# Performance work log

Hardware: AMD Instinct MI355X
Metric: run time of the kernel (lower is better)

The kernel has to match this reference:

```python
import jax, jax.numpy as jnp
import numpy as np

B, T, D, H, K, V, W = 2, 2048, 1024, 16, 64, 64, 256
BANK = 64
CUE = 50250
EPS = 1e-6
SCALE = K ** -0.5
LOCAL_SCALE = 0.3
ROPE_BASE = 10000.0


def setup_inputs() -> dict:
    key = jax.random.key(0)
    ks = jax.random.split(key, 13)
    s = 0.02
    return {
        "x": jax.random.normal(ks[0], (B, T, D), jnp.float32),
        "gdn_state": jax.random.normal(ks[1], (B, H, K, V), jnp.float32),
        "input_ids": jax.random.randint(ks[2], (B, T), 0, 50320),
        "key_bank": jax.random.normal(ks[3], (H, BANK, K), jnp.float32),
        "norm_w": jnp.ones((D,), jnp.float32),
        "wq": jax.random.normal(ks[4], (D, D), jnp.float32) * s,
        "wk": jax.random.normal(ks[5], (D, D), jnp.float32) * s,
        "wv": jax.random.normal(ks[6], (D, D), jnp.float32) * s,
        "wo": jax.random.normal(ks[7], (D, D), jnp.float32) * s,
        "w_gq": jax.random.normal(ks[8], (H * K, D), jnp.float32) * s,
        "w_ro": jax.random.normal(ks[9], (D, H * V), jnp.float32) * s,
        "w_gate": jax.random.normal(ks[10], (H, D), jnp.float32) * s,
        "b_gate": jnp.ones((H,), jnp.float32),
    }


def _rope(u):
    # u: [B, T, H, K]
    inv_freq = 1.0 / (ROPE_BASE ** (jnp.arange(0, K, 2, dtype=jnp.float32) / K))
    t = jnp.arange(T, dtype=jnp.float32)
    freqs = t[:, None] * inv_freq[None, :]            # [T, K/2]
    emb = jnp.concatenate([freqs, freqs], axis=-1)    # [T, K]
    cos = jnp.cos(emb)[None, :, None, :]
    sin = jnp.sin(emb)[None, :, None, :]
    u1, u2 = u[..., : K // 2], u[..., K // 2 :]
    rotated = jnp.concatenate([-u2, u1], axis=-1)
    return u * cos + rotated * sin


def reference(x, gdn_state, input_ids, key_bank, norm_w, wq, wk, wv, wo,
              w_gq, w_ro, w_gate, b_gate):
    # RMSNorm
    rms = jnp.sqrt(jnp.mean(x * x, axis=-1, keepdims=True) + EPS)
    x_norm = x / rms * norm_w

    # QKV projections -> [B, T, H, K]
    q = (x_norm @ wq.T).reshape(B, T, H, K)
    k = (x_norm @ wk.T).reshape(B, T, H, K)
    v = (x_norm @ wv.T).reshape(B, T, H, K)
    q = _rope(q)
    k = _rope(k)

    # Causal sliding-window attention (PyTorch fallback math: full TxT + band mask)
    scores = jnp.einsum("bthk,bshk->bhts", q, k) * SCALE  # [B, H, T, T]
    i = jnp.arange(T)
    allowed = (i[None, :] <= i[:, None]) & (i[None, :] >= i[:, None] - W)  # [T, T]
    scores = jnp.where(allowed[None, None], scores, jnp.float32(-jnp.inf))
    probs = jax.nn.softmax(scores, axis=-1)
    local = jnp.einsum("bhts,bshv->bthv", probs, v).reshape(B, T, D)
    local = LOCAL_SCALE * (local @ wo.T)  # eval path: local_scale * o_proj(local_out)

    # Global retrieval from GDN state
    q_g = (x_norm @ w_gq.T).reshape(B, T, H, K)
    # CUE token override: positions with input_ids == CUE + idx use key_bank[:, idx, :]
    idx = input_ids - CUE                              # [B, T]
    valid = (idx >= 0) & (idx < BANK)
    ci = jnp.clip(idx, 0, BANK - 1)
    gathered = key_bank.transpose(1, 0, 2)[ci]         # [B, T, H, K]
    q_g = jnp.where(valid[..., None, None], gathered, q_g)

    retrieved = jnp.einsum("bhkv,bthk->bthv", gdn_state, q_g).reshape(B, T, H * V)
    retrieval_out = retrieved @ w_ro.T                 # [B, T, D]
    gate = jax.nn.sigmoid(x_norm @ w_gate.T + b_gate)  # [B, T, H]
    retrieval_out = jnp.mean(gate, axis=-1, keepdims=True) * retrieval_out

    return x + local + retrieval_out
```

## Files before the change

kernel.cpp:

```cpp
#include <hip/hip_runtime.h>
#include <cstddef>

typedef __bf16 bf16_t;
typedef __bf16 bf16x8 __attribute__((ext_vector_type(8)));
typedef __bf16 bf16x4 __attribute__((ext_vector_type(4)));
typedef float  f32x4  __attribute__((ext_vector_type(4)));

__global__ __launch_bounds__(256) void rmsnorm_kernel(const float* __restrict__ x,
                                                      const float* __restrict__ w,
                                                      bf16_t* __restrict__ xn) {
  int t = blockIdx.x;
  int tid = threadIdx.x;
  const f32x4* row = (const f32x4*)(x + (size_t)t * 1024);
  f32x4 v = row[tid];
  float ss = v[0]*v[0] + v[1]*v[1] + v[2]*v[2] + v[3]*v[3];
  #pragma unroll
  for (int off = 32; off >= 1; off >>= 1) ss += __shfl_xor(ss, off);
  __shared__ float red[4];
  int wave = tid >> 6;
  if ((tid & 63) == 0) red[wave] = ss;
  __syncthreads();
  float tot = red[0] + red[1] + red[2] + red[3];
  float rinv = rsqrtf(tot * (1.0f / 1024.0f) + 1e-6f);
  f32x4 wv = ((const f32x4*)w)[tid];
  bf16x4 o;
  #pragma unroll
  for (int i = 0; i < 4; ++i) o[i] = (bf16_t)(v[i] * rinv * wv[i]);
  *(bf16x4*)(xn + (size_t)t * 1024 + tid * 4) = o;
}

struct CvtArgs { const float* s[6]; bf16_t* d[6]; };
__global__ __launch_bounds__(256) void convert6(CvtArgs a) {
  const f32x4* src = (const f32x4*)a.s[blockIdx.y];
  bf16_t* dst = a.d[blockIdx.y];
  int i = blockIdx.x * 256 + threadIdx.x;
  f32x4 v = src[i];
  bf16x4 o;
  #pragma unroll
  for (int j = 0; j < 4; ++j) o[j] = (bf16_t)v[j];
  *(bf16x4*)(dst + (size_t)i * 4) = o;
}

struct GemmSeg { const bf16_t* a; const bf16_t* w; void* c; };
struct GemmCfg { GemmSeg seg[4]; int bf16out; };
#define LDSK 40
__global__ __launch_bounds__(256, 2) void gemm_bt(GemmCfg cfg) {
  __shared__ bf16_t As[128 * LDSK];
  __shared__ bf16_t Bs[128 * LDSK];
  int seg = blockIdx.x >> 3;
  const bf16_t* __restrict__ A = cfg.seg[seg].a;
  const bf16_t* __restrict__ W = cfg.seg[seg].w;
  int m0 = blockIdx.y * 128;
  int n0 = (blockIdx.x & 7) * 128;
  int tid = threadIdx.x;
  int lane = tid & 63, wave = tid >> 6;
  int wm = (wave >> 1) * 64, wn = (wave & 1) * 64;
  int l16 = lane & 15, quad = lane >> 4;
  f32x4 acc[4][4] = {};
  for (int k0 = 0; k0 < 1024; k0 += 32) {
    __syncthreads();
    #pragma unroll
    for (int c = 0; c < 2; ++c) {
      int ci = tid + c * 256;
      int r = ci >> 2;
      int ko = (ci & 3) * 8;
      *(uint4*)&As[r * LDSK + ko] = *(const uint4*)&A[(size_t)(m0 + r) * 1024 + k0 + ko];
      *(uint4*)&Bs[r * LDSK + ko] = *(const uint4*)&W[(size_t)(n0 + r) * 1024 + k0 + ko];
    }
    __syncthreads();
    bf16x8 af[4], bfr[4];
    #pragma unroll
    for (int i = 0; i < 4; ++i) {
      af[i]  = *(const bf16x8*)&As[(wm + i * 16 + l16) * LDSK + quad * 8];
      bfr[i] = *(const bf16x8*)&Bs[(wn + i * 16 + l16) * LDSK + quad * 8];
    }
    #pragma unroll
    for (int i = 0; i < 4; ++i)
      #pragma unroll
      for (int j = 0; j < 4; ++j)
        acc[i][j] = __builtin_amdgcn_mfma_f32_16x16x32_bf16(af[i], bfr[j], acc[i][j], 0, 0, 0);
  }
  if (cfg.bf16out) {
    bf16_t* C = (bf16_t*)cfg.seg[seg].c;
    #pragma unroll
    for (int i = 0; i < 4; ++i)
      #pragma unroll
      for (int j = 0; j < 4; ++j) {
        int row = m0 + wm + i * 16 + quad * 4;
        int col = n0 + wn + j * 16 + l16;
        #pragma unroll
        for (int r = 0; r < 4; ++r)
          C[(size_t)(row + r) * 1024 + col] = (bf16_t)acc[i][j][r];
      }
  } else {
    float* C = (float*)cfg.seg[seg].c;
    #pragma unroll
    for (int i = 0; i < 4; ++i)
      #pragma unroll
      for (int j = 0; j < 4; ++j) {
        int row = m0 + wm + i * 16 + quad * 4;
        int col = n0 + wn + j * 16 + l16;
        #pragma unroll
        for (int r = 0; r < 4; ++r)
          C[(size_t)(row + r) * 1024 + col] = acc[i][j][r];
      }
  }
}

__global__ __launch_bounds__(256) void rope_kernel(bf16_t* __restrict__ q,
                                                   bf16_t* __restrict__ k) {
  int idx = blockIdx.x * 256 + threadIdx.x;
  int d = idx & 31;
  int h = (idx >> 5) & 15;
  int t = (idx >> 9) & 2047;
  int b = idx >> 20;
  float inv = expf((float)d * (-2.0f / 64.0f) * 9.210340371976184f);
  float f = (float)t * inv;
  float sn, cs;
  sincosf(f, &sn, &cs);
  size_t base = (((size_t)(b * 2048 + t) * 16) + h) * 64;
  float q1 = (float)q[base + d], q2 = (float)q[base + d + 32];
  q[base + d]      = (bf16_t)(q1 * cs - q2 * sn);
  q[base + d + 32] = (bf16_t)(q2 * cs + q1 * sn);
  float k1 = (float)k[base + d], k2 = (float)k[base + d + 32];
  k[base + d]      = (bf16_t)(k1 * cs - k2 * sn);
  k[base + d + 32] = (bf16_t)(k2 * cs + k1 * sn);
}

__global__ __launch_bounds__(256) void attn_mfma(const bf16_t* __restrict__ qb,
                                                 const bf16_t* __restrict__ kb,
                                                 const bf16_t* __restrict__ vb,
                                                 bf16_t* __restrict__ ob) {
  __shared__ bf16_t Ks[64 * 72];
  __shared__ bf16_t Vt[64 * 72];
  __shared__ float  Os[4][16 * 68];
  int blk = blockIdx.x;
  int tcb = blk & 31;
  int h = (blk >> 5) & 15;
  int b = blk >> 9;
  int t0 = tcb * 64;
  int tid = threadIdx.x;
  int wv = tid >> 6, lane = tid & 63;
  int l15 = lane & 15, quad = lane >> 4;
  int tq0 = t0 + wv * 16;
  int t = tq0 + l15;
  int lo = t - 256; if (lo < 0) lo = 0;

  const bf16_t* qptr = qb + (((size_t)(b * 2048 + t) * 16) + h) * 64;
  bf16x8 qf0 = *(const bf16x8*)(qptr + quad * 8);
  bf16x8 qf1 = *(const bf16x8*)(qptr + 32 + quad * 8);

  f32x4 acc[4] = {};
  float mrun = -1e30f, lrun = 0.f;

  for (int c = 0; c < 5; ++c) {
    int s0 = t0 - 256 + c * 64;
    __syncthreads();
    #pragma unroll
    for (int it = 0; it < 2; ++it) {
      int task = tid + it * 256;
      int key = task >> 3, dseg = task & 7;
      int s = s0 + key; s = s < 0 ? 0 : (s > 2047 ? 2047 : s);
      *(bf16x8*)&Ks[key * 72 + dseg * 8] =
        *(const bf16x8*)(kb + (((size_t)(b * 2048 + s) * 16) + h) * 64 + dseg * 8);
    }
    {
      int vseg = tid & 7, kp = tid >> 3;
      int sA = s0 + 2 * kp, sB = sA + 1;
      sA = sA < 0 ? 0 : (sA > 2047 ? 2047 : sA);
      sB = sB < 0 ? 0 : (sB > 2047 ? 2047 : sB);
      bf16x8 va = *(const bf16x8*)(vb + (((size_t)(b * 2048 + sA) * 16) + h) * 64 + vseg * 8);
      bf16x8 vbv = *(const bf16x8*)(vb + (((size_t)(b * 2048 + sB) * 16) + h) * 64 + vseg * 8);
      #pragma unroll
      for (int j = 0; j < 8; ++j) {
        union { bf16_t h2[2]; unsigned int u; } pk;
        pk.h2[0] = va[j]; pk.h2[1] = vbv[j];
        *(unsigned int*)&Vt[(vseg * 8 + j) * 72 + 2 * kp] = pk.u;
      }
    }
    __syncthreads();
    #pragma unroll
    for (int p = 0; p < 2; ++p) {
      int sbase = s0 + p * 32;
      if (sbase > tq0 + 15 || sbase + 31 < tq0 - 256 || sbase + 31 < 0) continue;
      int kl = p * 32;
      bf16x8 ka0  = *(const bf16x8*)&Ks[(kl + l15) * 72 + quad * 8];
      bf16x8 ka0b = *(const bf16x8*)&Ks[(kl + l15) * 72 + 32 + quad * 8];
      bf16x8 ka1  = *(const bf16x8*)&Ks[(kl + 16 + l15) * 72 + quad * 8];
      bf16x8 ka1b = *(const bf16x8*)&Ks[(kl + 16 + l15) * 72 + 32 + quad * 8];
      f32x4 c0 = {}, c1 = {};
      c0 = __builtin_amdgcn_mfma_f32_16x16x32_bf16(ka0,  qf0, c0, 0, 0, 0);
      c0 = __builtin_amdgcn_mfma_f32_16x16x32_bf16(ka0b, qf1, c0, 0, 0, 0);
      c1 = __builtin_amdgcn_mfma_f32_16x16x32_bf16(ka1,  qf0, c1, 0, 0, 0);
      c1 = __builtin_amdgcn_mfma_f32_16x16x32_bf16(ka1b, qf1, c1, 0, 0, 0);
      float p0[4], p1[4];
      float mx = -1e30f;
      #pragma unroll
      for (int r = 0; r < 4; ++r) {
        int sK0 = sbase + quad * 4 + r;
        int sK1 = sK0 + 16;
        float v0 = (sK0 >= lo && sK0 <= t) ? c0[r] * 0.125f : -1e30f;
        float v1 = (sK1 >= lo && sK1 <= t) ? c1[r] * 0.125f : -1e30f;
        p0[r] = v0; p1[r] = v1;
        mx = fmaxf(mx, fmaxf(v0, v1));
      }
      mx = fmaxf(mx, __shfl_xor(mx, 16));
      mx = fmaxf(mx, __shfl_xor(mx, 32));
      float mnew = fmaxf(mrun, mx);
      float alpha = __expf(mrun - mnew);
      float rs = 0.f;
      #pragma unroll
      for (int r = 0; r < 4; ++r) {
        float e0 = (p0[r] > -1e29f) ? __expf(p0[r] - mnew) : 0.f;
        float e1 = (p1[r] > -1e29f) ? __expf(p1[r] - mnew) : 0.f;
        p0[r] = e0; p1[r] = e1;
        rs += e0 + e1;
      }
      rs += __shfl_xor(rs, 16);
      rs += __shfl_xor(rs, 32);
      mrun = mnew;
      lrun = lrun * alpha + rs;
      #pragma unroll
      for (int vt = 0; vt < 4; ++vt)
        #pragma unroll
        for (int r = 0; r < 4; ++r) acc[vt][r] *= alpha;
      union { bf16x4 v; int2 i2; } pka, pkb;
      #pragma unroll
      for (int r = 0; r < 4; ++r) { pka.v[r] = (bf16_t)p0[r]; pkb.v[r] = (bf16_t)p1[r]; }
      int sel = quad >> 1;
      int base = l15 + ((quad & 1) << 5);
      int a0 = __shfl(pka.i2.x, base),      b0 = __shfl(pkb.i2.x, base);
      int a1 = __shfl(pka.i2.y, base),      b1 = __shfl(pkb.i2.y, base);
      int a2 = __shfl(pka.i2.x, base + 16), b2 = __shfl(pkb.i2.x, base + 16);
      int a3 = __shfl(pka.i2.y, base + 16), b3 = __shfl(pkb.i2.y, base + 16);
      union { int4 i4; bf16x8 v; } pf;
      pf.i4.x = sel ? b0 : a0;
      pf.i4.y = sel ? b1 : a1;
      pf.i4.z = sel ? b2 : a2;
      pf.i4.w = sel ? b3 : a3;
      #pragma unroll
      for (int vt = 0; vt < 4; ++vt) {
        bf16x8 vfr = *(const bf16x8*)&Vt[(vt * 16 + l15) * 72 + kl + quad * 8];
        acc[vt] = __builtin_amdgcn_mfma_f32_16x16x32_bf16(vfr, pf.v, acc[vt], 0, 0, 0);
      }
    }
  }
  float rl = 1.0f / lrun;
  float* myOs = &Os[wv][0];
  #pragma unroll
  for (int vt = 0; vt < 4; ++vt)
    #pragma unroll
    for (int r = 0; r < 4; ++r)
      myOs[l15 * 68 + vt * 16 + quad * 4 + r] = acc[vt][r] * rl;
  __syncthreads();
  #pragma unroll
  for (int q = 0; q < 16; ++q) {
    float v = myOs[q * 68 + lane];
    ob[(((size_t)(b * 2048 + tq0 + q) * 16) + h) * 64 + lane] = (bf16_t)v;
  }
}

__global__ __launch_bounds__(256, 4) void gate_kernel(const bf16_t* __restrict__ xn,
                                                      const float* __restrict__ wg,
                                                      const float* __restrict__ bg,
                                                      float* __restrict__ gm) {
  int wave = threadIdx.x >> 6, lane = threadIdx.x & 63;
  int t = blockIdx.x * 4 + wave;
  float acc[16];
  #pragma unroll
  for (int h = 0; h < 16; ++h) acc[h] = 0.f;
  const bf16_t* xr = xn + (size_t)t * 1024;
  for (int i = 0; i < 16; ++i) {
    float xv = (float)xr[i * 64 + lane];
    #pragma unroll
    for (int h = 0; h < 16; ++h) acc[h] += xv * wg[h * 1024 + i * 64 + lane];
  }
  #pragma unroll
  for (int h = 0; h < 16; ++h) {
    float s = acc[h];
    #pragma unroll
    for (int off = 32; off >= 1; off >>= 1) s += __shfl_xor(s, off);
    acc[h] = s;
  }
  if (lane == 0) {
    float g = 0.f;
    #pragma unroll
    for (int h = 0; h < 16; ++h) g += 1.0f / (1.0f + __expf(-(acc[h] + bg[h])));
    gm[t] = g * (1.0f / 16.0f);
  }
}

__global__ __launch_bounds__(256, 2) void retrieval_kernel(const bf16_t* __restrict__ qgb,
                                                           const int* __restrict__ ids,
                                                           const float* __restrict__ bank,
                                                           const float* __restrict__ gdn,
                                                           bf16_t* __restrict__ rb) {
  __shared__ float G[64 * 64];
  int blk = blockIdx.x;
  int tc = blk & 7;
  int h = (blk >> 3) & 15;
  int b = blk >> 7;
  int tid = threadIdx.x;
  const f32x4* gsrc = (const f32x4*)(gdn + (size_t)(b * 16 + h) * 4096);
  #pragma unroll
  for (int it = 0; it < 4; ++it)
    ((f32x4*)G)[tid + it * 256] = gsrc[tid + it * 256];
  __syncthreads();
  int t = tc * 256 + tid;
  int id = ids[b * 2048 + t] - 50250;
  bool valid = (id >= 0) && (id < 64);
  const bf16_t* qrow = qgb + (((size_t)(b * 2048 + t) * 16) + h) * 64;
  const float* krow = bank + (size_t)(h * 64 + (valid ? id : 0)) * 64;
  float acc[64];
  #pragma unroll
  for (int v = 0; v < 64; ++v) acc[v] = 0.f;
  for (int k = 0; k < 64; ++k) {
    float qv = valid ? krow[k] : (float)qrow[k];
    const f32x4* gr = (const f32x4*)&G[k * 64];
    #pragma unroll
    for (int i = 0; i < 16; ++i) {
      f32x4 gv = gr[i];
      acc[i * 4 + 0] += qv * gv[0];
      acc[i * 4 + 1] += qv * gv[1];
      acc[i * 4 + 2] += qv * gv[2];
      acc[i * 4 + 3] += qv * gv[3];
    }
  }
  bf16_t* orow = rb + (((size_t)(b * 2048 + t) * 16) + h) * 64;
  #pragma unroll
  for (int i = 0; i < 8; ++i) {
    bf16x8 ov;
    #pragma unroll
    for (int j = 0; j < 8; ++j) ov[j] = (bf16_t)acc[i * 8 + j];
    *(bf16x8*)(orow + i * 8) = ov;
  }
}

__global__ __launch_bounds__(256) void final_kernel(const float* __restrict__ x,
                                                    const bf16_t* __restrict__ lb,
                                                    const bf16_t* __restrict__ rbuf,
                                                    const float* __restrict__ gm,
                                                    float* __restrict__ out) {
  int i = blockIdx.x * 256 + threadIdx.x;
  float g = gm[i >> 7];
  bf16x8 lv = ((const bf16x8*)lb)[i];
  bf16x8 rv = ((const bf16x8*)rbuf)[i];
  const f32x4* xr = (const f32x4*)x;
  f32x4 x0 = xr[i * 2], x1 = xr[i * 2 + 1];
  f32x4 o0, o1;
  #pragma unroll
  for (int j = 0; j < 4; ++j) {
    o0[j] = x0[j] + 0.3f * (float)lv[j]     + g * (float)rv[j];
    o1[j] = x1[j] + 0.3f * (float)lv[j + 4] + g * (float)rv[j + 4];
  }
  f32x4* od = (f32x4*)out;
  od[i * 2] = o0;
  od[i * 2 + 1] = o1;
}

extern "C" void kernel_launch(void* const* d_in, const int* in_sizes, int n_in,
                              void* d_out, int out_size, void* d_ws, size_t ws_size,
                              hipStream_t stream) {
  const float* x        = (const float*)d_in[0];
  const float* gdn      = (const float*)d_in[1];
  const int*   ids      = (const int*)d_in[2];
  const float* key_bank = (const float*)d_in[3];
  const float* norm_w   = (const float*)d_in[4];
  const float* wq       = (const float*)d_in[5];
  const float* wk       = (const float*)d_in[6];
  const float* wv       = (const float*)d_in[7];
  const float* wo       = (const float*)d_in[8];
  const float* w_gq     = (const float*)d_in[9];
  const float* w_ro     = (const float*)d_in[10];
  const float* w_gate   = (const float*)d_in[11];
  const float* b_gate   = (const float*)d_in[12];

  char* p = (char*)d_ws;
  auto alloc = [&](size_t bytes) { char* r = p; p += (bytes + 255) & ~(size_t)255; return r; };
  const size_t ACT = (size_t)4096 * 1024 * 2;
  const size_t WTB = (size_t)1024 * 1024 * 2;
  bf16_t* xn_b   = (bf16_t*)alloc(ACT);
  bf16_t* wq_b   = (bf16_t*)alloc(WTB);
  bf16_t* wk_b   = (bf16_t*)alloc(WTB);
  bf16_t* wv_b   = (bf16_t*)alloc(WTB);
  bf16_t* wo_b   = (bf16_t*)alloc(WTB);
  bf16_t* wgq_b  = (bf16_t*)alloc(WTB);
  bf16_t* wro_b  = (bf16_t*)alloc(WTB);
  bf16_t* qb     = (bf16_t*)alloc(ACT);
  bf16_t* kb     = (bf16_t*)alloc(ACT);
  bf16_t* vb     = (bf16_t*)alloc(ACT);
  bf16_t* qgb    = (bf16_t*)alloc(ACT);
  bf16_t* attn_b = (bf16_t*)alloc(ACT);
  bf16_t* retr_b = (bf16_t*)alloc(ACT);
  bf16_t* local_b= (bf16_t*)alloc(ACT);
  bf16_t* retro_b= (bf16_t*)alloc(ACT);
  float*  gmean  = (float*)alloc(4096 * 4);

  CvtArgs ca;
  ca.s[0] = wq;   ca.d[0] = wq_b;
  ca.s[1] = wk;   ca.d[1] = wk_b;
  ca.s[2] = wv;   ca.d[2] = wv_b;
  ca.s[3] = wo;   ca.d[3] = wo_b;
  ca.s[4] = w_gq; ca.d[4] = wgq_b;
  ca.s[5] = w_ro; ca.d[5] = wro_b;
  convert6<<<dim3(1024, 6), 256, 0, stream>>>(ca);
  rmsnorm_kernel<<<4096, 256, 0, stream>>>(x, norm_w, xn_b);

  GemmCfg g4;
  g4.seg[0] = {xn_b, wq_b,  (void*)qb};
  g4.seg[1] = {xn_b, wk_b,  (void*)kb};
  g4.seg[2] = {xn_b, wv_b,  (void*)vb};
  g4.seg[3] = {xn_b, wgq_b, (void*)qgb};
  g4.bf16out = 1;
  gemm_bt<<<dim3(32, 32), 256, 0, stream>>>(g4);

  rope_kernel<<<8192, 256, 0, stream>>>(qb, kb);
  attn_mfma<<<1024, 256, 0, stream>>>(qb, kb, vb, attn_b);
  gate_kernel<<<1024, 256, 0, stream>>>(xn_b, w_gate, b_gate, gmean);
  retrieval_kernel<<<256, 256, 0, stream>>>(qgb, ids, key_bank, gdn, retr_b);

  GemmCfg g2;
  g2.seg[0] = {attn_b, wo_b,  (void*)local_b};
  g2.seg[1] = {retr_b, wro_b, (void*)retro_b};
  g2.seg[2] = g2.seg[0];
  g2.seg[3] = g2.seg[0];
  g2.bf16out = 1;
  gemm_bt<<<dim3(16, 32), 256, 0, stream>>>(g2);

  final_kernel<<<2048, 256, 0, stream>>>(x, local_b, retro_b, gmean, (float*)d_out);
}
```

Measured before the change: 263.4 us.

## Fuse RoPE, gate, and residual epilogue into GEMMs; concatenate output projections

Folds RoPE into the QKV GEMM epilogue and the gate projection into the RMSNorm kernel. The attention and gated retrieval outputs are concatenated along K so that one GEMM against a concatenated [wo*0.3 | w_ro] weight produces the final output, adding x in its epilogue. This removes the rope, gate and final kernels and several intermediate activation round-trips. It also switches GEMM tile loads to direct global-to-LDS loads without padding, which may add LDS bank conflicts. The final GEMM launches only 256 blocks with K=2048, which may underfill the GPU.

```diff
diff --git a/kernel.cpp b/kernel.cpp
--- a/kernel.cpp
+++ b/kernel.cpp
@@ -6,73 +6,107 @@
 typedef __bf16 bf16x4 __attribute__((ext_vector_type(4)));
 typedef float  f32x4  __attribute__((ext_vector_type(4)));
 
-__global__ __launch_bounds__(256) void rmsnorm_kernel(const float* __restrict__ x,
-                                                      const float* __restrict__ w,
-                                                      bf16_t* __restrict__ xn) {
+typedef const __attribute__((address_space(1))) void* gas_p;
+typedef __attribute__((address_space(3))) void* las_p;
+__device__ __forceinline__ void gload16(const bf16_t* g, bf16_t* l) {
+  __builtin_amdgcn_global_load_lds((gas_p)g, (las_p)l, 16, 0, 0);
+}
+
+__global__ __launch_bounds__(256) void rmsnorm_gate(const float* __restrict__ x,
+                                                    const float* __restrict__ w,
+                                                    const float* __restrict__ wg,
+                                                    const float* __restrict__ bg,
+                                                    bf16_t* __restrict__ xn,
+                                                    float* __restrict__ gm) {
   int t = blockIdx.x;
   int tid = threadIdx.x;
+  int wave = tid >> 6, lane = tid & 63;
   const f32x4* row = (const f32x4*)(x + (size_t)t * 1024);
   f32x4 v = row[tid];
   float ss = v[0]*v[0] + v[1]*v[1] + v[2]*v[2] + v[3]*v[3];
   #pragma unroll
   for (int off = 32; off >= 1; off >>= 1) ss += __shfl_xor(ss, off);
   __shared__ float red[4];
-  int wave = tid >> 6;
-  if ((tid & 63) == 0) red[wave] = ss;
+  __shared__ float gred[4][16];
+  if (lane == 0) red[wave] = ss;
   __syncthreads();
   float tot = red[0] + red[1] + red[2] + red[3];
   float rinv = rsqrtf(tot * (1.0f / 1024.0f) + 1e-6f);
   f32x4 wv = ((const f32x4*)w)[tid];
+  float xnv[4];
   bf16x4 o;
   #pragma unroll
-  for (int i = 0; i < 4; ++i) o[i] = (bf16_t)(v[i] * rinv * wv[i]);
+  for (int i = 0; i < 4; ++i) { xnv[i] = v[i] * rinv * wv[i]; o[i] = (bf16_t)xnv[i]; }
   *(bf16x4*)(xn + (size_t)t * 1024 + tid * 4) = o;
-}
-
-struct CvtArgs { const float* s[6]; bf16_t* d[6]; };
+  float ga[16];
+  #pragma unroll
+  for (int h = 0; h < 16; ++h) {
+    f32x4 wgh = ((const f32x4*)(wg + h * 1024))[tid];
+    ga[h] = xnv[0]*wgh[0] + xnv[1]*wgh[1] + xnv[2]*wgh[2] + xnv[3]*wgh[3];
+  }
+  #pragma unroll
+  for (int h = 0; h < 16; ++h) {
+    #pragma unroll
+    for (int off = 32; off >= 1; off >>= 1) ga[h] += __shfl_xor(ga[h], off);
+  }
+  if (lane < 16) gred[wave][lane] = ga[lane];
+  __syncthreads();
+  if (tid < 16) {
+    float s = gred[0][tid] + gred[1][tid] + gred[2][tid] + gred[3][tid];
+    float sig = 1.0f / (1.0f + __expf(-(s + bg[tid])));
+    #pragma unroll
+    for (int off = 8; off >= 1; off >>= 1) sig += __shfl_xor(sig, off);
+    if (tid == 0) gm[t] = sig * (1.0f / 16.0f);
+  }
+}
+
+struct CvtArgs { const float* s[6]; bf16_t* d[6]; int stride[6]; float scale[6]; };
 __global__ __launch_bounds__(256) void convert6(CvtArgs a) {
-  const f32x4* src = (const f32x4*)a.s[blockIdx.y];
-  bf16_t* dst = a.d[blockIdx.y];
+  int m = blockIdx.y;
+  const f32x4* src = (const f32x4*)a.s[m];
   int i = blockIdx.x * 256 + threadIdx.x;
   f32x4 v = src[i];
+  int rrow = i >> 8;
+  int col = (i & 255) * 4;
+  float sc = a.scale[m];
   bf16x4 o;
   #pragma unroll
-  for (int j = 0; j < 4; ++j) o[j] = (bf16_t)v[j];
-  *(bf16x4*)(dst + (size_t)i * 4) = o;
-}
-
-struct GemmSeg { const bf16_t* a; const bf16_t* w; void* c; };
-struct GemmCfg { GemmSeg seg[4]; int bf16out; };
-#define LDSK 40
+  for (int j = 0; j < 4; ++j) o[j] = (bf16_t)(v[j] * sc);
+  *(bf16x4*)(a.d[m] + (size_t)rrow * a.stride[m] + col) = o;
+}
+
+struct GemmSeg { const bf16_t* a; const bf16_t* w; void* c; int mode; };
+struct GemmCfg { GemmSeg seg[4]; int Kd; const float* x; };
 __global__ __launch_bounds__(256, 2) void gemm_bt(GemmCfg cfg) {
-  __shared__ bf16_t As[128 * LDSK];
-  __shared__ bf16_t Bs[128 * LDSK];
+  __shared__ bf16_t As[128 * 32];
+  __shared__ bf16_t Bs[128 * 32];
   int seg = blockIdx.x >> 3;
   const bf16_t* __restrict__ A = cfg.seg[seg].a;
   const bf16_t* __restrict__ W = cfg.seg[seg].w;
+  int Kd = cfg.Kd;
   int m0 = blockIdx.y * 128;
   int n0 = (blockIdx.x & 7) * 128;
   int tid = threadIdx.x;
   int lane = tid & 63, wave = tid >> 6;
   int wm = (wave >> 1) * 64, wn = (wave & 1) * 64;
   int l16 = lane & 15, quad = lane >> 4;
+  const bf16_t* agp = A + (size_t)(m0 + wave * 32 + (lane >> 2)) * Kd + (lane & 3) * 8;
+  const bf16_t* wgp = W + (size_t)(n0 + wave * 32 + (lane >> 2)) * Kd + (lane & 3) * 8;
+  bf16_t* alds = &As[wave * 32 * 32];
+  bf16_t* blds = &Bs[wave * 32 * 32];
   f32x4 acc[4][4] = {};
-  for (int k0 = 0; k0 < 1024; k0 += 32) {
+  for (int k0 = 0; k0 < Kd; k0 += 32) {
     __syncthreads();
-    #pragma unroll
-    for (int c = 0; c < 2; ++c) {
-      int ci = tid + c * 256;
-      int r = ci >> 2;
-      int ko = (ci & 3) * 8;
-      *(uint4*)&As[r * LDSK + ko] = *(const uint4*)&A[(size_t)(m0 + r) * 1024 + k0 + ko];
-      *(uint4*)&Bs[r * LDSK + ko] = *(const uint4*)&W[(size_t)(n0 + r) * 1024 + k0 + ko];
-    }
+    gload16(agp + k0,               alds);
+    gload16(agp + k0 + 16 * Kd,     alds + 16 * 32);
+    gload16(wgp + k0,               blds);
+    gload16(wgp + k0 + 16 * Kd,     blds + 16 * 32);
     __syncthreads();
     bf16x8 af[4], bfr[4];
     #pragma unroll
     for (int i = 0; i < 4; ++i) {
-      af[i]  = *(const bf16x8*)&As[(wm + i * 16 + l16) * LDSK + quad * 8];
-      bfr[i] = *(const bf16x8*)&Bs[(wn + i * 16 + l16) * LDSK + quad * 8];
+      af[i]  = *(const bf16x8*)&As[(wm + i * 16 + l16) * 32 + quad * 8];
+      bfr[i] = *(const bf16x8*)&Bs[(wn + i * 16 + l16) * 32 + quad * 8];
     }
     #pragma unroll
     for (int i = 0; i < 4; ++i)
@@ -80,7 +114,41 @@
       for (int j = 0; j < 4; ++j)
         acc[i][j] = __builtin_amdgcn_mfma_f32_16x16x32_bf16(af[i], bfr[j], acc[i][j], 0, 0, 0);
   }
-  if (cfg.bf16out) {
+  int mode = cfg.seg[seg].mode;
+  if (mode == 1) {
+    #pragma unroll
+    for (int jp = 0; jp < 2; ++jp) {
+      int d = jp * 16 + l16;
+      float inv = exp2f((float)d * -0.41524101186092029f);
+      #pragma unroll
+      for (int i = 0; i < 4; ++i)
+        #pragma unroll
+        for (int r = 0; r < 4; ++r) {
+          int tseq = (m0 + wm + i * 16 + quad * 4 + r) & 2047;
+          float sn, cs;
+          sincosf((float)tseq * inv, &sn, &cs);
+          float v1 = acc[i][jp][r], v2 = acc[i][jp + 2][r];
+          acc[i][jp][r]     = v1 * cs - v2 * sn;
+          acc[i][jp + 2][r] = v2 * cs + v1 * sn;
+        }
+    }
+  }
+  if (mode == 2) {
+    float* C = (float*)cfg.seg[seg].c;
+    const float* X = cfg.x;
+    #pragma unroll
+    for (int i = 0; i < 4; ++i)
+      #pragma unroll
+      for (int j = 0; j < 4; ++j) {
+        int row = m0 + wm + i * 16 + quad * 4;
+        int col = n0 + wn + j * 16 + l16;
+        #pragma unroll
+        for (int r = 0; r < 4; ++r) {
+          size_t idx = (size_t)(row + r) * 1024 + col;
+          C[idx] = X[idx] + acc[i][j][r];
+        }
+      }
+  } else {
     bf16_t* C = (bf16_t*)cfg.seg[seg].c;
     #pragma unroll
     for (int i = 0; i < 4; ++i)
@@ -92,45 +160,13 @@
         for (int r = 0; r < 4; ++r)
           C[(size_t)(row + r) * 1024 + col] = (bf16_t)acc[i][j][r];
       }
-  } else {
-    float* C = (float*)cfg.seg[seg].c;
-    #pragma unroll
-    for (int i = 0; i < 4; ++i)
-      #pragma unroll
-      for (int j = 0; j < 4; ++j) {
-        int row = m0 + wm + i * 16 + quad * 4;
-        int col = n0 + wn + j * 16 + l16;
-        #pragma unroll
-        for (int r = 0; r < 4; ++r)
-          C[(size_t)(row + r) * 1024 + col] = acc[i][j][r];
-      }
-  }
-}
-
-__global__ __launch_bounds__(256) void rope_kernel(bf16_t* __restrict__ q,
-                                                   bf16_t* __restrict__ k) {
-  int idx = blockIdx.x * 256 + threadIdx.x;
-  int d = idx & 31;
-  int h = (idx >> 5) & 15;
-  int t = (idx >> 9) & 2047;
-  int b = idx >> 20;
-  float inv = expf((float)d * (-2.0f / 64.0f) * 9.210340371976184f);
-  float f = (float)t * inv;
-  float sn, cs;
-  sincosf(f, &sn, &cs);
-  size_t base = (((size_t)(b * 2048 + t) * 16) + h) * 64;
-  float q1 = (float)q[base + d], q2 = (float)q[base + d + 32];
-  q[base + d]      = (bf16_t)(q1 * cs - q2 * sn);
-  q[base + d + 32] = (bf16_t)(q2 * cs + q1 * sn);
-  float k1 = (float)k[base + d], k2 = (float)k[base + d + 32];
-  k[base + d]      = (bf16_t)(k1 * cs - k2 * sn);
-  k[base + d + 32] = (bf16_t)(k2 * cs + k1 * sn);
+  }
 }
 
 __global__ __launch_bounds__(256) void attn_mfma(const bf16_t* __restrict__ qb,
                                                  const bf16_t* __restrict__ kb,
                                                  const bf16_t* __restrict__ vb,
-                                                 bf16_t* __restrict__ ob) {
+                                                 bf16_t* __restrict__ ab2) {
   __shared__ bf16_t Ks[64 * 72];
   __shared__ bf16_t Vt[64 * 72];
   __shared__ float  Os[4][16 * 68];
@@ -256,37 +292,7 @@
   #pragma unroll
   for (int q = 0; q < 16; ++q) {
     float v = myOs[q * 68 + lane];
-    ob[(((size_t)(b * 2048 + tq0 + q) * 16) + h) * 64 + lane] = (bf16_t)v;
-  }
-}
-
-__global__ __launch_bounds__(256, 4) void gate_kernel(const bf16_t* __restrict__ xn,
-                                                      const float* __restrict__ wg,
-                                                      const float* __restrict__ bg,
-                                                      float* __restrict__ gm) {
-  int wave = threadIdx.x >> 6, lane = threadIdx.x & 63;
-  int t = blockIdx.x * 4 + wave;
-  float acc[16];
-  #pragma unroll
-  for (int h = 0; h < 16; ++h) acc[h] = 0.f;
-  const bf16_t* xr = xn + (size_t)t * 1024;
-  for (int i = 0; i < 16; ++i) {
-    float xv = (float)xr[i * 64 + lane];
-    #pragma unroll
-    for (int h = 0; h < 16; ++h) acc[h] += xv * wg[h * 1024 + i * 64 + lane];
-  }
-  #pragma unroll
-  for (int h = 0; h < 16; ++h) {
-    float s = acc[h];
-    #pragma unroll
-    for (int off = 32; off >= 1; off >>= 1) s += __shfl_xor(s, off);
-    acc[h] = s;
-  }
-  if (lane == 0) {
-    float g = 0.f;
-    #pragma unroll
-    for (int h = 0; h < 16; ++h) g += 1.0f / (1.0f + __expf(-(acc[h] + bg[h])));
-    gm[t] = g * (1.0f / 16.0f);
+    ab2[(size_t)(b * 2048 + tq0 + q) * 2048 + h * 64 + lane] = (bf16_t)v;
   }
 }
 
@@ -294,7 +300,8 @@
                                                            const int* __restrict__ ids,
                                                            const float* __restrict__ bank,
                                                            const float* __restrict__ gdn,
-                                                           bf16_t* __restrict__ rb) {
+                                                           const float* __restrict__ gm,
+                                                           bf16_t* __restrict__ ab2) {
   __shared__ float G[64 * 64];
   int blk = blockIdx.x;
   int tc = blk & 7;
@@ -326,36 +333,15 @@
       acc[i * 4 + 3] += qv * gv[3];
     }
   }
-  bf16_t* orow = rb + (((size_t)(b * 2048 + t) * 16) + h) * 64;
+  float g = gm[b * 2048 + t];
+  bf16_t* orow = ab2 + (size_t)(b * 2048 + t) * 2048 + 1024 + h * 64;
   #pragma unroll
   for (int i = 0; i < 8; ++i) {
     bf16x8 ov;
     #pragma unroll
-    for (int j = 0; j < 8; ++j) ov[j] = (bf16_t)acc[i * 8 + j];
+    for (int j = 0; j < 8; ++j) ov[j] = (bf16_t)(acc[i * 8 + j] * g);
     *(bf16x8*)(orow + i * 8) = ov;
   }
-}
-
-__global__ __launch_bounds__(256) void final_kernel(const float* __restrict__ x,
-                                                    const bf16_t* __restrict__ lb,
-                                                    const bf16_t* __restrict__ rbuf,
-                                                    const float* __restrict__ gm,
-                                                    float* __restrict__ out) {
-  int i = blockIdx.x * 256 + threadIdx.x;
-  float g = gm[i >> 7];
-  bf16x8 lv = ((const bf16x8*)lb)[i];
-  bf16x8 rv = ((const bf16x8*)rbuf)[i];
-  const f32x4* xr = (const f32x4*)x;
-  f32x4 x0 = xr[i * 2], x1 = xr[i * 2 + 1];
-  f32x4 o0, o1;
-  #pragma unroll
-  for (int j = 0; j < 4; ++j) {
-    o0[j] = x0[j] + 0.3f * (float)lv[j]     + g * (float)rv[j];
-    o1[j] = x1[j] + 0.3f * (float)lv[j + 4] + g * (float)rv[j + 4];
-  }
-  f32x4* od = (f32x4*)out;
-  od[i * 2] = o0;
-  od[i * 2 + 1] = o1;
 }
 
 extern "C" void kernel_launch(void* const* d_in, const int* in_sizes, int n_in,
@@ -383,49 +369,43 @@
   bf16_t* wq_b   = (bf16_t*)alloc(WTB);
   bf16_t* wk_b   = (bf16_t*)alloc(WTB);
   bf16_t* wv_b   = (bf16_t*)alloc(WTB);
-  bf16_t* wo_b   = (bf16_t*)alloc(WTB);
   bf16_t* wgq_b  = (bf16_t*)alloc(WTB);
-  bf16_t* wro_b  = (bf16_t*)alloc(WTB);
+  bf16_t* wcat   = (bf16_t*)alloc(WTB * 2);
   bf16_t* qb     = (bf16_t*)alloc(ACT);
   bf16_t* kb     = (bf16_t*)alloc(ACT);
   bf16_t* vb     = (bf16_t*)alloc(ACT);
   bf16_t* qgb    = (bf16_t*)alloc(ACT);
-  bf16_t* attn_b = (bf16_t*)alloc(ACT);
-  bf16_t* retr_b = (bf16_t*)alloc(ACT);
-  bf16_t* local_b= (bf16_t*)alloc(ACT);
-  bf16_t* retro_b= (bf16_t*)alloc(ACT);
+  bf16_t* ab2    = (bf16_t*)alloc(ACT * 2);
   float*  gmean  = (float*)alloc(4096 * 4);
 
   CvtArgs ca;
-  ca.s[0] = wq;   ca.d[0] = wq_b;
-  ca.s[1] = wk;   ca.d[1] = wk_b;
-  ca.s[2] = wv;   ca.d[2] = wv_b;
-  ca.s[3] = wo;   ca.d[3] = wo_b;
-  ca.s[4] = w_gq; ca.d[4] = wgq_b;
-  ca.s[5] = w_ro; ca.d[5] = wro_b;
+  ca.s[0] = wq;   ca.d[0] = wq_b;        ca.stride[0] = 1024; ca.scale[0] = 1.0f;
+  ca.s[1] = wk;   ca.d[1] = wk_b;        ca.stride[1] = 1024; ca.scale[1] = 1.0f;
+  ca.s[2] = wv;   ca.d[2] = wv_b;        ca.stride[2] = 1024; ca.scale[2] = 1.0f;
+  ca.s[3] = w_gq; ca.d[3] = wgq_b;       ca.stride[3] = 1024; ca.scale[3] = 1.0f;
+  ca.s[4] = wo;   ca.d[4] = wcat;        ca.stride[4] = 2048; ca.scale[4] = 0.3f;
+  ca.s[5] = w_ro; ca.d[5] = wcat + 1024; ca.stride[5] = 2048; ca.scale[5] = 1.0f;
   convert6<<<dim3(1024, 6), 256, 0, stream>>>(ca);
-  rmsnorm_kernel<<<4096, 256, 0, stream>>>(x, norm_w, xn_b);
+  rmsnorm_gate<<<4096, 256, 0, stream>>>(x, norm_w, w_gate, b_gate, xn_b, gmean);
 
   GemmCfg g4;
-  g4.seg[0] = {xn_b, wq_b,  (void*)qb};
-  g4.seg[1] = {xn_b, wk_b,  (void*)kb};
-  g4.seg[2] = {xn_b, wv_b,  (void*)vb};
-  g4.seg[3] = {xn_b, wgq_b, (void*)qgb};
-  g4.bf16out = 1;
+  g4.seg[0] = {xn_b, wq_b,  (void*)qb,  1};
+  g4.seg[1] = {xn_b, wk_b,  (void*)kb,  1};
+  g4.seg[2] = {xn_b, wv_b,  (void*)vb,  0};
+  g4.seg[3] = {xn_b, wgq_b, (void*)qgb, 0};
+  g4.Kd = 1024;
+  g4.x = nullptr;
   gemm_bt<<<dim3(32, 32), 256, 0, stream>>>(g4);
 
-  rope_kernel<<<8192, 256, 0, stream>>>(qb, kb);
-  attn_mfma<<<1024, 256, 0, stream>>>(qb, kb, vb, attn_b);
-  gate_kernel<<<1024, 256, 0, stream>>>(xn_b, w_gate, b_gate, gmean);
-  retrieval_kernel<<<256, 256, 0, stream>>>(qgb, ids, key_bank, gdn, retr_b);
-
-  GemmCfg g2;
-  g2.seg[0] = {attn_b, wo_b,  (void*)local_b};
-  g2.seg[1] = {retr_b, wro_b, (void*)retro_b};
-  g2.seg[2] = g2.seg[0];
-  g2.seg[3] = g2.seg[0];
-  g2.bf16out = 1;
-  gemm_bt<<<dim3(16, 32), 256, 0, stream>>>(g2);
-
-  final_kernel<<<2048, 256, 0, stream>>>(x, local_b, retro_b, gmean, (float*)d_out);
-}
+  attn_mfma<<<1024, 256, 0, stream>>>(qb, kb, vb, ab2);
+  retrieval_kernel<<<256, 256, 0, stream>>>(qgb, ids, key_bank, gdn, gmean, ab2);
+
+  GemmCfg gf;
+  gf.seg[0] = {ab2, wcat, d_out, 2};
+  gf.seg[1] = gf.seg[0];
+  gf.seg[2] = gf.seg[0];
+  gf.seg[3] = gf.seg[0];
+  gf.Kd = 2048;
+  gf.x = x;
+  gemm_bt<<<dim3(8, 32), 256, 0, stream>>>(gf);
+}
```

Result: slower. 285.3 us (+8.3%).
